# Kernel tuning notes

Measured on AMD Instinct MI355X. Metric: run time of the kernel, lower is better.

## Reference

```python
import jax, jax.numpy as jnp
import numpy as np

B, S, D = 4, 2048, 1024
H, DK, DV = 16, 64, 64
TEMP = (4 * DK) ** 0.5
EPS = 1e-6


def setup_inputs() -> dict:
    key = jax.random.key(0)
    ks = jax.random.split(key, 16)
    def lin(k, fin, fout):
        # torch Linear default init: U(-1/sqrt(fin), 1/sqrt(fin)); weight stored [fout,fin], we use [fin,fout]
        bound = 1.0 / np.sqrt(fin)
        return jax.random.uniform(k, (fin, fout), jnp.float32, -bound, bound)
    inp = {}
    for i, name in enumerate(['q_a', 'k_a', 'v_a', 'q_s', 'k_s', 'v_s']):
        inp[name] = jax.random.normal(ks[i], (B, S, D), jnp.float32)
    inp['Wqa'] = lin(ks[6], D, H * DK)
    inp['Wka'] = lin(ks[7], D, H * DK)
    inp['Wva'] = lin(ks[8], D, H * DV)
    inp['Wqs'] = lin(ks[9], D, H * DK)
    inp['Wks'] = lin(ks[10], D, H * DK)
    inp['Wvs'] = lin(ks[11], D, H * DV)
    inp['Wfc'] = lin(ks[12], H * DV, D)
    inp['gamma'] = jnp.ones((D,), jnp.float32)
    inp['beta'] = jnp.zeros((D,), jnp.float32)
    return inp


def _proj(x, W, dh):
    # [B,S,D] @ [D,H*dh] -> [B,H,S,dh]
    b, s, _ = x.shape
    return (x @ W).reshape(b, s, H, dh).transpose(0, 2, 1, 3)


def reference(q_a, k_a, v_a, q_s, k_s, v_s, Wqa, Wka, Wva, Wqs, Wks, Wvs, Wfc, gamma, beta):
    residual = q_a + q_s
    qa = _proj(q_a, Wqa, DK)
    ka = _proj(k_a, Wka, DK)
    va = _proj(v_a, Wva, DV)
    qs = _proj(q_s, Wqs, DK)
    ks = _proj(k_s, Wks, DK)
    vs = _proj(v_s, Wvs, DV)
    # a2a + a2s + s2a + s2s == (qa+qs) @ (ka+ks)^T  (same math, single GEMM)
    scores = jnp.einsum('bhqd,bhkd->bhqk', qa + qs, ka + ks) / TEMP
    attn = jax.nn.softmax(scores, axis=-1)  # [B,H,S,S]
    ctx = jnp.einsum('bhqk,bhkd->bhqd', attn, va + vs)
    ctx = ctx.transpose(0, 2, 1, 3).reshape(q_a.shape[0], q_a.shape[1], H * DV)
    out = ctx @ Wfc + residual
    mu = jnp.mean(out, axis=-1, keepdims=True)
    var = jnp.var(out, axis=-1, keepdims=True)
    out = (out - mu) * jax.lax.rsqrt(var + EPS) * gamma + beta
    return out
```

## Files before the change

### kernel.cpp

```cpp
#include <hip/hip_runtime.h>
#include <hip/hip_bf16.h>
#include <cstdint>
#include <cstddef>

typedef __bf16 bf16;
typedef __bf16 bf16x8 __attribute__((ext_vector_type(8)));
typedef __bf16 bf16x4v __attribute__((ext_vector_type(4)));
typedef __bf16 bf16x2v __attribute__((ext_vector_type(2)));
typedef float f32x4 __attribute__((ext_vector_type(4)));
typedef float f32x16 __attribute__((ext_vector_type(16)));
typedef unsigned uint2v __attribute__((ext_vector_type(2)));
typedef unsigned uint4v __attribute__((ext_vector_type(4)));

#define MFMA16(a, b, c) __builtin_amdgcn_mfma_f32_16x16x32_bf16((a), (b), (c), 0, 0, 0)
#define MFMA32(a, b, c) __builtin_amdgcn_mfma_f32_32x32x16_bf16((a), (b), (c), 0, 0, 0)
#define SWZ(row, byte) ((((row) * 128) + (byte)) ^ (((row) & 7) << 4))
#define GLOAD_LDS(g, l) \
    __builtin_amdgcn_global_load_lds((const __attribute__((address_space(1))) void*)(g), \
                                     (__attribute__((address_space(3))) void*)(l), 16, 0, 0)

constexpr int BB = 4, SS = 2048, DD = 1024, HH = 16;
constexpr int NROWS = BB * SS;
constexpr size_t NB = (size_t)NROWS * DD;
constexpr size_t NW = (size_t)DD * DD;

static __device__ __forceinline__ unsigned pk2(float a, float b) {
    bf16x2v h;
    h[0] = (bf16)a; h[1] = (bf16)b;
    return __builtin_bit_cast(unsigned, h);
}

static __device__ __forceinline__ bf16x8 frag4(unsigned w0, unsigned w1, unsigned w2, unsigned w3) {
    uint4v u;
    u[0] = w0; u[1] = w1; u[2] = w2; u[3] = w3;
    return __builtin_bit_cast(bf16x8, u);
}

struct Ptrs6 { const float* p[6]; };

__global__ __launch_bounds__(256) void cvt_in_kernel(Ptrs6 src, bf16* dst) {
    const int z = blockIdx.y;
    const size_t idx = (size_t)blockIdx.x * 256 + threadIdx.x;
    float4 v = ((const float4*)src.p[z])[idx];
    bf16x4v o;
    o[0] = (bf16)v.x; o[1] = (bf16)v.y; o[2] = (bf16)v.z; o[3] = (bf16)v.w;
    *(bf16x4v*)(dst + z * NB + idx * 4) = o;
}

struct Ptrs7 { const float* p[7]; };

__global__ __launch_bounds__(256) void cvt_w_kernel(Ptrs7 src, bf16* dst) {
    const int z = blockIdx.z;
    const float* W = src.p[z];
    bf16* WT = dst + (size_t)z * NW;
    __shared__ float tile[32][33];
    const int tx = threadIdx.x, ty = threadIdx.y;
    const int kb = blockIdx.y * 32, nb = blockIdx.x * 32;
#pragma unroll
    for (int j = 0; j < 4; ++j)
        tile[ty + j * 8][tx] = W[(size_t)(kb + ty + j * 8) * DD + nb + tx];
    __syncthreads();
#pragma unroll
    for (int j = 0; j < 4; ++j)
        WT[(size_t)(nb + ty + j * 8) * DD + kb + tx] = (bf16)tile[tx][ty + j * 8];
}

__global__ __launch_bounds__(256) void vt_kernel(const bf16* __restrict__ V,
                                                 bf16* __restrict__ Vt) {
    const int bh = blockIdx.y;
    const int s0 = blockIdx.x * 64;
    __shared__ bf16 t[64][72];
    const int tid = threadIdx.x;
    const int row = tid >> 2, seg = tid & 3;
    const bf16* src = V + ((size_t)bh * SS + s0 + row) * 64 + seg * 16;
    bf16x8 v0 = *(const bf16x8*)src;
    bf16x8 v1 = *(const bf16x8*)(src + 8);
#pragma unroll
    for (int j = 0; j < 8; ++j) {
        t[seg * 16 + j][row] = v0[j];
        t[seg * 16 + 8 + j][row] = v1[j];
    }
    __syncthreads();
    const int d = tid >> 2, c = (tid & 3) * 16;
    bf16x8 o0 = *(const bf16x8*)(&t[d][c]);
    bf16x8 o1 = *(const bf16x8*)(&t[d][c + 8]);
    bf16* dst = Vt + ((size_t)bh * 64 + d) * SS + s0 + c;
    *(bf16x8*)dst = o0;
    *(bf16x8*)(dst + 8) = o1;
}

struct GemmPtrs {
    const bf16* a1[3]; const bf16* a2[3];
    const bf16* b1[3]; const bf16* b2[3];
    bf16* outbh[3];
};

template <int MODE>
__global__ __launch_bounds__(256) void gemm_kernel(GemmPtrs P, int iters, int split,
                                                   float* outF, const float* r1, const float* r2) {
    const int cpx = gridDim.x >> 3;
    const int bid0 = blockIdx.x;
    const int work = (bid0 & 7) * cpx + (bid0 >> 3);
    const int z = work >> 9;
    const int rem = work & 511;
    const int m0 = (rem >> 3) * 128, n0 = (rem & 7) * 128;

    const bf16* __restrict__ A1 = P.a1[z];
    const bf16* __restrict__ A2 = P.a2[z];
    const bf16* __restrict__ B1 = P.b1[z];
    const bf16* __restrict__ B2 = P.b2[z];

    const int tid = threadIdx.x;
    const int lane = tid & 63, w = tid >> 6;
    const int g = lane >> 4, i = lane & 15;
    const int mb = (w >> 1) * 64, nb = (w & 1) * 64;

    __shared__ __align__(16) bf16 As[128 * 64];
    __shared__ __align__(16) bf16 Bs[128 * 64];

    const int lrow = lane >> 3, lseg = lane & 7;
    const int chunk = lseg ^ lrow;

    f32x4 acc[4][4];
#pragma unroll
    for (int aa = 0; aa < 4; ++aa)
#pragma unroll
        for (int bb = 0; bb < 4; ++bb) acc[aa][bb] = 0.0f;

    for (int kt = 0; kt < iters; ++kt) {
        const bf16* Ag; const bf16* Bg; int koff;
        if (kt < split) { Ag = A1; Bg = B1; koff = kt * 64; }
        else            { Ag = A2; Bg = B2; koff = (kt - split) * 64; }

        __syncthreads();
#pragma unroll
        for (int c = 0; c < 4; ++c) {
            const int row = (w * 4 + c) * 8 + lrow;
            const bf16* ap;
            if (MODE == 0) {
                ap = Ag + (size_t)(m0 + row) * DD + koff + chunk * 8;
            } else {
                int gr = m0 + row;
                ap = Ag + ((size_t)((gr >> 11) * HH + (koff >> 6)) * SS + (gr & 2047)) * 64 + chunk * 8;
            }
            const bf16* bp = Bg + (size_t)(n0 + row) * DD + koff + chunk * 8;
            GLOAD_LDS(ap, As + (w * 4 + c) * 512);
            GLOAD_LDS(bp, Bs + (w * 4 + c) * 512);
        }
        __syncthreads();

#pragma unroll
        for (int f = 0; f < 2; ++f) {
            bf16x8 af[4], bff[4];
#pragma unroll
            for (int mt = 0; mt < 4; ++mt) {
                int row = mb + mt * 16 + i;
                af[mt] = *(const bf16x8*)((char*)As + SWZ(row, f * 64 + g * 16));
            }
#pragma unroll
            for (int nt = 0; nt < 4; ++nt) {
                int row = nb + nt * 16 + i;
                bff[nt] = *(const bf16x8*)((char*)Bs + SWZ(row, f * 64 + g * 16));
            }
#pragma unroll
            for (int mt = 0; mt < 4; ++mt)
#pragma unroll
                for (int nt = 0; nt < 4; ++nt)
                    acc[mt][nt] = MFMA16(af[mt], bff[nt], acc[mt][nt]);
        }
    }

    if (MODE == 0) {
        bf16* outQ = P.outbh[z];
#pragma unroll
        for (int mt = 0; mt < 4; ++mt)
#pragma unroll
            for (int nt = 0; nt < 4; ++nt) {
                int colg = n0 + nb + nt * 16 + i;
                int h = colg >> 6, d = colg & 63;
#pragma unroll
                for (int r = 0; r < 4; ++r) {
                    int rowg = m0 + mb + mt * 16 + g * 4 + r;
                    int b = rowg >> 11, s = rowg & 2047;
                    outQ[(((size_t)(b * HH + h)) * SS + s) * 64 + d] = (bf16)acc[mt][nt][r];
                }
            }
    } else {
#pragma unroll
        for (int mt = 0; mt < 4; ++mt)
#pragma unroll
            for (int nt = 0; nt < 4; ++nt) {
                int colg = n0 + nb + nt * 16 + i;
#pragma unroll
                for (int r = 0; r < 4; ++r) {
                    int rowg = m0 + mb + mt * 16 + g * 4 + r;
                    size_t off = (size_t)rowg * DD + colg;
                    outF[off] = acc[mt][nt][r] + r1[off] + r2[off];
                }
            }
    }
}

__global__ __launch_bounds__(512, 4) void attn_kernel(const bf16* __restrict__ Qg,
                                                      const bf16* __restrict__ Kg,
                                                      const bf16* __restrict__ Vt,
                                                      bf16* __restrict__ ctxh) {
    const int bid = blockIdx.x;
    const int bh = ((bid & 7) << 3) | (bid >> 6);
    const int qt = (bid >> 3) & 7;

    const int tid = threadIdx.x;
    const int lane = tid & 63, w = tid >> 6;
    const int hi = lane >> 5, q = lane & 31;

    __shared__ __align__(16) char smem[32768];

    const int qrow = qt * 256 + w * 32 + q;
    bf16x8 qf[4];
    {
        const bf16* qp = Qg + ((size_t)bh * SS + qrow) * 64;
#pragma unroll
        for (int c = 0; c < 4; ++c) {
            bf16x8 v = *(const bf16x8*)(qp + c * 16 + hi * 8);
#pragma unroll
            for (int e = 0; e < 8; ++e) v[e] = (bf16)((float)v[e] * 0.0625f);
            qf[c] = v;
        }
    }

    const int srow = tid >> 3, sseg = tid & 7;
    const bf16* kgp = Kg + (size_t)bh * SS * 64;
    const bf16* vgp = Vt + (size_t)bh * 64 * SS;
    const int sbyte = SWZ(srow, sseg * 16);

    bf16x8 kreg = *(const bf16x8*)(kgp + (size_t)srow * 64 + sseg * 8);
    bf16x8 vreg = *(const bf16x8*)(vgp + (size_t)srow * SS + sseg * 8);

    f32x16 o0 = {}, o1 = {};
    float m = -3e38f, l = 0.0f;

    for (int kt = 0; kt < SS / 64; ++kt) {
        char* kb_ = smem + (kt & 1) * 16384;
        char* vb_ = kb_ + 8192;
        *(bf16x8*)(kb_ + sbyte) = kreg;
        *(bf16x8*)(vb_ + sbyte) = vreg;
        if (kt + 1 < SS / 64) {
            const int k0n = (kt + 1) * 64;
            kreg = *(const bf16x8*)(kgp + (size_t)(k0n + srow) * 64 + sseg * 8);
            vreg = *(const bf16x8*)(vgp + (size_t)srow * SS + k0n + sseg * 8);
        }
        __syncthreads();

        f32x16 st0 = {}, st1 = {};
        __builtin_amdgcn_s_setprio(1);
#pragma unroll
        for (int c = 0; c < 4; ++c) {
            bf16x8 kf = *(const bf16x8*)(kb_ + SWZ(q, c * 32 + hi * 16));
            st0 = MFMA32(kf, qf[c], st0);
        }
#pragma unroll
        for (int c = 0; c < 4; ++c) {
            bf16x8 kf = *(const bf16x8*)(kb_ + SWZ(32 + q, c * 32 + hi * 16));
            st1 = MFMA32(kf, qf[c], st1);
        }
        __builtin_amdgcn_s_setprio(0);

        float tm = st0[0];
#pragma unroll
        for (int r = 1; r < 16; ++r) tm = fmaxf(tm, st0[r]);
#pragma unroll
        for (int r = 0; r < 16; ++r) tm = fmaxf(tm, st1[r]);
        tm = fmaxf(tm, __shfl_xor(tm, 32, 64));
        if (!__all(tm - m <= 8.0f)) {
            float nm = fmaxf(m, tm);
            float al = __expf(m - nm);
            l *= al;
            o0 *= al;
            o1 *= al;
            m = nm;
        }
        float sum = 0.0f;
#pragma unroll
        for (int r = 0; r < 16; ++r) { st0[r] = __expf(st0[r] - m); sum += st0[r]; }
#pragma unroll
        for (int r = 0; r < 16; ++r) { st1[r] = __expf(st1[r] - m); sum += st1[r]; }
        l += sum;

        bf16x8 pf[4];
#pragma unroll
        for (int c = 0; c < 4; ++c) {
            const f32x16 s_ = (c < 2) ? st0 : st1;
            const int b0 = (c & 1) * 8;
            unsigned a0 = pk2(s_[b0 + 0], s_[b0 + 1]);
            unsigned c0 = pk2(s_[b0 + 4], s_[b0 + 5]);
            unsigned a1 = pk2(s_[b0 + 2], s_[b0 + 3]);
            unsigned c1 = pk2(s_[b0 + 6], s_[b0 + 7]);
            uint2v s1 = __builtin_amdgcn_permlane32_swap(a0, c0, false, false);
            uint2v s2 = __builtin_amdgcn_permlane32_swap(a1, c1, false, false);
            pf[c] = frag4(s1[0], s2[0], s1[1], s2[1]);
        }

        __builtin_amdgcn_s_setprio(1);
#pragma unroll
        for (int c = 0; c < 4; ++c) {
            bf16x8 vf = *(const bf16x8*)(vb_ + SWZ(q, c * 32 + hi * 16));
            o0 = MFMA32(vf, pf[c], o0);
        }
#pragma unroll
        for (int c = 0; c < 4; ++c) {
            bf16x8 vf = *(const bf16x8*)(vb_ + SWZ(32 + q, c * 32 + hi * 16));
            o1 = MFMA32(vf, pf[c], o1);
        }
        __builtin_amdgcn_s_setprio(0);
    }

    float lt = l + __shfl_xor(l, 32, 64);
    float rl = 1.0f / lt;
    __syncthreads();
    const int orow = w * 32 + q;
#pragma unroll
    for (int dh = 0; dh < 2; ++dh) {
#pragma unroll
        for (int r = 0; r < 16; r += 2) {
            float v0 = (dh ? o1[r] : o0[r]) * rl;
            float v1 = (dh ? o1[r + 1] : o0[r + 1]) * rl;
            int d = dh * 32 + (r & 3) + 8 * (r >> 2) + 4 * hi;
            *(unsigned*)(smem + SWZ(orow, d * 2)) = pk2(v0, v1);
        }
    }
    __syncthreads();
    {
        const int row = tid >> 1, hf = tid & 1;
        bf16* outp = ctxh + ((size_t)bh * SS + qt * 256 + row) * 64 + hf * 32;
#pragma unroll
        for (int c = 0; c < 4; ++c) {
            bf16x8 v = *(const bf16x8*)(smem + SWZ(row, hf * 64 + c * 16));
            *(bf16x8*)(outp + c * 8) = v;
        }
    }
}

__global__ __launch_bounds__(256) void ln_kernel(const float* __restrict__ tmp,
                                                 const float* __restrict__ gamma,
                                                 const float* __restrict__ beta,
                                                 float* __restrict__ out) {
    const int row = blockIdx.x;
    const int t = threadIdx.x;
    float4 v = ((const float4*)(tmp + (size_t)row * DD))[t];
    float s = v.x + v.y + v.z + v.w;
    float ss = v.x * v.x + v.y * v.y + v.z * v.z + v.w * v.w;
#pragma unroll
    for (int mask = 1; mask <= 32; mask <<= 1) {
        s += __shfl_xor(s, mask, 64);
        ss += __shfl_xor(ss, mask, 64);
    }
    __shared__ float red[8];
    const int w = t >> 6, lane = t & 63;
    if (lane == 0) { red[w] = s; red[4 + w] = ss; }
    __syncthreads();
    s = red[0] + red[1] + red[2] + red[3];
    ss = red[4] + red[5] + red[6] + red[7];
    const float mu = s * (1.0f / 1024.0f);
    const float var = ss * (1.0f / 1024.0f) - mu * mu;
    const float rs = rsqrtf(var + 1e-6f);
    float4 gm = ((const float4*)gamma)[t];
    float4 bt = ((const float4*)beta)[t];
    float4 ov;
    ov.x = (v.x - mu) * rs * gm.x + bt.x;
    ov.y = (v.y - mu) * rs * gm.y + bt.y;
    ov.z = (v.z - mu) * rs * gm.z + bt.z;
    ov.w = (v.w - mu) * rs * gm.w + bt.w;
    ((float4*)(out + (size_t)row * DD))[t] = ov;
}

extern "C" void kernel_launch(void* const* d_in, const int* in_sizes, int n_in,
                              void* d_out, int out_size, void* d_ws, size_t ws_size,
                              hipStream_t stream) {
    (void)in_sizes; (void)n_in; (void)out_size; (void)ws_size;

    char* ws = (char*)d_ws;
    bf16* xb = (bf16*)ws;
    bf16* wT = (bf16*)(ws + 100663296ull);
    bf16* Qg = (bf16*)(ws + 115343360ull);
    bf16* Kg = (bf16*)(ws + 132120576ull);
    bf16* Vg = (bf16*)(ws + 148897792ull);
    bf16* ctxh = (bf16*)ws;
    bf16* Vtg = (bf16*)(ws + 16777216ull);
    float* tmp = (float*)(ws + 33554432ull);

    {
        Ptrs6 p;
        for (int j = 0; j < 6; ++j) p.p[j] = (const float*)d_in[j];
        cvt_in_kernel<<<dim3(8192, 6), 256, 0, stream>>>(p, xb);
    }
    {
        Ptrs7 p;
        for (int j = 0; j < 7; ++j) p.p[j] = (const float*)d_in[6 + j];
        cvt_w_kernel<<<dim3(32, 32, 7), dim3(32, 8), 0, stream>>>(p, wT);
    }
    {
        GemmPtrs gp;
        gp.a1[0] = xb;           gp.a1[1] = xb + NB;     gp.a1[2] = xb + 2 * NB;
        gp.a2[0] = xb + 3 * NB;  gp.a2[1] = xb + 4 * NB; gp.a2[2] = xb + 5 * NB;
        gp.b1[0] = wT;           gp.b1[1] = wT + NW;     gp.b1[2] = wT + 2 * NW;
        gp.b2[0] = wT + 3 * NW;  gp.b2[1] = wT + 4 * NW; gp.b2[2] = wT + 5 * NW;
        gp.outbh[0] = Qg; gp.outbh[1] = Kg; gp.outbh[2] = Vg;
        gemm_kernel<0><<<dim3(1536), 256, 0, stream>>>(gp, 32, 16, nullptr, nullptr, nullptr);
    }
    vt_kernel<<<dim3(32, 64), 256, 0, stream>>>(Vg, Vtg);
    attn_kernel<<<dim3(512), 512, 0, stream>>>(Qg, Kg, Vtg, ctxh);
    {
        GemmPtrs gp;
        for (int j = 0; j < 3; ++j) {
            gp.a1[j] = ctxh; gp.a2[j] = ctxh;
            gp.b1[j] = wT + 6 * NW; gp.b2[j] = wT + 6 * NW;
            gp.outbh[j] = nullptr;
        }
        gemm_kernel<1><<<dim3(512), 256, 0, stream>>>(gp, 16, 16, tmp,
                                                      (const float*)d_in[0],
                                                      (const float*)d_in[3]);
    }
    ln_kernel<<<dim3(8192), 256, 0, stream>>>(tmp, (const float*)d_in[13],
                                              (const float*)d_in[14], (float*)d_out);
}
```

Measured before the change: 533.0 us.

## Replace QKV projection GEMM with 256x256-tile double-buffered 8-wave kernel

Replaces the 128x128-tile projection GEMM (1536 blocks of 256 threads) with a new 256x256-tile kernel (384 blocks of 512 threads). The new kernel stages A and B through 128 KB of double-buffered LDS with direct global-to-LDS loads and splits each K step into four phases. Each phase interleaves the next tile's loads with MFMA bursts, using explicit waitcnt, barriers and setprio. The larger tile cuts global and LDS traffic per FLOP, but the 128 KB of LDS per block and the many barriers limit occupancy, and 384 blocks may fill the CUs unevenly.

```diff
diff --git a/kernel.cpp b/kernel.cpp
--- a/kernel.cpp
+++ b/kernel.cpp
@@ -18,6 +18,10 @@
 #define GLOAD_LDS(g, l) \
     __builtin_amdgcn_global_load_lds((const __attribute__((address_space(1))) void*)(g), \
                                      (__attribute__((address_space(3))) void*)(l), 16, 0, 0)
+#define VMWAIT(n) asm volatile("s_waitcnt vmcnt(" #n ")" ::: "memory")
+#define LGKM0()   asm volatile("s_waitcnt lgkmcnt(0)" ::: "memory")
+#define BAR()     __builtin_amdgcn_s_barrier()
+#define SCHED0()  __builtin_amdgcn_sched_barrier(0)
 
 constexpr int BB = 4, SS = 2048, DD = 1024, HH = 16;
 constexpr int NROWS = BB * SS;
@@ -94,6 +98,164 @@
     const bf16* b1[3]; const bf16* b2[3];
     bf16* outbh[3];
 };
+
+__global__ __launch_bounds__(512, 2) void gemm256_kernel(GemmPtrs P) {
+    const int tid = threadIdx.x;
+    const int lane = tid & 63, w = tid >> 6;
+    const int g = lane >> 4, i = lane & 15;
+    const int chunk = (tid & 7) ^ ((tid >> 3) & 7);
+
+    const int cpx = gridDim.x >> 3;
+    const int work = (blockIdx.x & 7) * cpx + (blockIdx.x >> 3);
+    const int mpanel = work / 12;
+    const int ntile = work - mpanel * 12;
+    const int z = ntile >> 2;
+    const int n0 = (ntile & 3) * 256;
+    const int m0 = mpanel * 256;
+
+    const bf16* __restrict__ A1 = P.a1[z];
+    const bf16* __restrict__ A2 = P.a2[z];
+    const bf16* __restrict__ B1 = P.b1[z];
+    const bf16* __restrict__ B2 = P.b2[z];
+
+    __shared__ __align__(16) char smem[131072];
+
+    f32x4 acc[16][2];
+#pragma unroll
+    for (int a = 0; a < 16; ++a) { acc[a][0] = 0.0f; acc[a][1] = 0.0f; }
+
+    auto stage = [&](char* region, const bf16* G, int rc0, int rbase, int ko) {
+        GLOAD_LDS(G + (size_t)(rc0 + rbase + (tid >> 3)) * 1024 + ko + chunk * 8,
+                  region + rbase * 128 + w * 1024);
+    };
+
+#define LDFRAG(base, row, byte) (*(const bf16x8*)((base) + SWZ((row), (byte))))
+#define LDB_ALL(Bb) do { \
+    bf_[0][0] = LDFRAG((Bb), w * 32 + i,      g * 16); \
+    bf_[0][1] = LDFRAG((Bb), w * 32 + i,      64 + g * 16); \
+    bf_[1][0] = LDFRAG((Bb), w * 32 + 16 + i, g * 16); \
+    bf_[1][1] = LDFRAG((Bb), w * 32 + 16 + i, 64 + g * 16); } while (0)
+#define LDA_PH(Ab, q) do { \
+    af_[0][0] = LDFRAG((Ab), (q) * 64 + i,      g * 16); \
+    af_[0][1] = LDFRAG((Ab), (q) * 64 + i,      64 + g * 16); \
+    af_[1][0] = LDFRAG((Ab), (q) * 64 + 16 + i, g * 16); \
+    af_[1][1] = LDFRAG((Ab), (q) * 64 + 16 + i, 64 + g * 16); \
+    af_[2][0] = LDFRAG((Ab), (q) * 64 + 32 + i, g * 16); \
+    af_[2][1] = LDFRAG((Ab), (q) * 64 + 32 + i, 64 + g * 16); \
+    af_[3][0] = LDFRAG((Ab), (q) * 64 + 48 + i, g * 16); \
+    af_[3][1] = LDFRAG((Ab), (q) * 64 + 48 + i, 64 + g * 16); } while (0)
+#define MFMA_PH(q) do { \
+    __builtin_amdgcn_s_setprio(1); \
+    acc[(q)*4+0][0] = MFMA16(af_[0][0], bf_[0][0], acc[(q)*4+0][0]); \
+    acc[(q)*4+0][0] = MFMA16(af_[0][1], bf_[0][1], acc[(q)*4+0][0]); \
+    acc[(q)*4+0][1] = MFMA16(af_[0][0], bf_[1][0], acc[(q)*4+0][1]); \
+    acc[(q)*4+0][1] = MFMA16(af_[0][1], bf_[1][1], acc[(q)*4+0][1]); \
+    acc[(q)*4+1][0] = MFMA16(af_[1][0], bf_[0][0], acc[(q)*4+1][0]); \
+    acc[(q)*4+1][0] = MFMA16(af_[1][1], bf_[0][1], acc[(q)*4+1][0]); \
+    acc[(q)*4+1][1] = MFMA16(af_[1][0], bf_[1][0], acc[(q)*4+1][1]); \
+    acc[(q)*4+1][1] = MFMA16(af_[1][1], bf_[1][1], acc[(q)*4+1][1]); \
+    acc[(q)*4+2][0] = MFMA16(af_[2][0], bf_[0][0], acc[(q)*4+2][0]); \
+    acc[(q)*4+2][0] = MFMA16(af_[2][1], bf_[0][1], acc[(q)*4+2][0]); \
+    acc[(q)*4+2][1] = MFMA16(af_[2][0], bf_[1][0], acc[(q)*4+2][1]); \
+    acc[(q)*4+2][1] = MFMA16(af_[2][1], bf_[1][1], acc[(q)*4+2][1]); \
+    acc[(q)*4+3][0] = MFMA16(af_[3][0], bf_[0][0], acc[(q)*4+3][0]); \
+    acc[(q)*4+3][0] = MFMA16(af_[3][1], bf_[0][1], acc[(q)*4+3][0]); \
+    acc[(q)*4+3][1] = MFMA16(af_[3][0], bf_[1][0], acc[(q)*4+3][1]); \
+    acc[(q)*4+3][1] = MFMA16(af_[3][1], bf_[1][1], acc[(q)*4+3][1]); \
+    __builtin_amdgcn_s_setprio(0); } while (0)
+
+    stage(smem + 65536, B1, n0, 0, 0);
+    stage(smem + 65536, B1, n0, 64, 0);
+    stage(smem + 65536, B1, n0, 128, 0);
+    stage(smem + 65536, B1, n0, 192, 0);
+    stage(smem, A1, m0, 0, 0);
+    stage(smem, A1, m0, 64, 0);
+    stage(smem, A1, m0, 128, 0);
+    stage(smem, A1, m0, 192, 0);
+    VMWAIT(3);
+    BAR();
+
+    bf16x8 bf_[2][2], af_[4][2];
+
+    for (int t = 0; t < 31; ++t) {
+        const int cur = t & 1;
+        char* Ab = smem + cur * 32768;
+        char* Bb = smem + 65536 + cur * 32768;
+        char* An_ = smem + (cur ^ 1) * 32768;
+        char* Bn_ = smem + 65536 + (cur ^ 1) * 32768;
+        const int ts = t + 1;
+        const bf16* Ag; const bf16* Bg; int ko;
+        if (ts < 16) { Ag = A1; Bg = B1; ko = ts * 64; }
+        else         { Ag = A2; Bg = B2; ko = (ts - 16) * 64; }
+
+        LDB_ALL(Bb);
+        LDA_PH(Ab, 0);
+        stage(Bn_, Bg, n0, 0, ko);
+        stage(Bn_, Bg, n0, 64, ko);
+        VMWAIT(4); BAR(); LGKM0(); SCHED0();
+        MFMA_PH(0);
+        BAR();
+        LDA_PH(Ab, 1);
+        stage(Bn_, Bg, n0, 128, ko);
+        stage(Bn_, Bg, n0, 192, ko);
+        VMWAIT(5); BAR(); LGKM0(); SCHED0();
+        MFMA_PH(1);
+        BAR();
+        LDA_PH(Ab, 2);
+        stage(An_, Ag, m0, 0, ko);
+        stage(An_, Ag, m0, 64, ko);
+        VMWAIT(6); BAR(); LGKM0(); SCHED0();
+        MFMA_PH(2);
+        BAR();
+        LDA_PH(Ab, 3);
+        stage(An_, Ag, m0, 128, ko);
+        stage(An_, Ag, m0, 192, ko);
+        VMWAIT(3); BAR(); LGKM0(); SCHED0();
+        MFMA_PH(3);
+        BAR();
+    }
+
+    {
+        char* Ab = smem + 32768;
+        char* Bb = smem + 65536 + 32768;
+        LDB_ALL(Bb);
+        LDA_PH(Ab, 0);
+        VMWAIT(2); BAR(); LGKM0(); SCHED0();
+        MFMA_PH(0);
+        BAR();
+        LDA_PH(Ab, 1);
+        VMWAIT(1); BAR(); LGKM0(); SCHED0();
+        MFMA_PH(1);
+        BAR();
+        LDA_PH(Ab, 2);
+        VMWAIT(0); BAR(); LGKM0(); SCHED0();
+        MFMA_PH(2);
+        BAR();
+        LDA_PH(Ab, 3);
+        LGKM0(); SCHED0();
+        MFMA_PH(3);
+    }
+
+    bf16* outQ = P.outbh[z];
+#pragma unroll
+    for (int mt = 0; mt < 16; ++mt) {
+#pragma unroll
+        for (int nt = 0; nt < 2; ++nt) {
+            int c = n0 + w * 32 + nt * 16 + i;
+            int h = c >> 6, d = c & 63;
+#pragma unroll
+            for (int r = 0; r < 4; ++r) {
+                int rowg = m0 + mt * 16 + g * 4 + r;
+                int b = rowg >> 11, s = rowg & 2047;
+                outQ[(((size_t)(b * HH + h)) * SS + s) * 64 + d] = (bf16)acc[mt][nt][r];
+            }
+        }
+    }
+#undef LDFRAG
+#undef LDB_ALL
+#undef LDA_PH
+#undef MFMA_PH
+}
 
 template <int MODE>
 __global__ __launch_bounds__(256) void gemm_kernel(GemmPtrs P, int iters, int split,
@@ -405,7 +567,7 @@
         gp.b1[0] = wT;           gp.b1[1] = wT + NW;     gp.b1[2] = wT + 2 * NW;
         gp.b2[0] = wT + 3 * NW;  gp.b2[1] = wT + 4 * NW; gp.b2[2] = wT + 5 * NW;
         gp.outbh[0] = Qg; gp.outbh[1] = Kg; gp.outbh[2] = Vg;
-        gemm_kernel<0><<<dim3(1536), 256, 0, stream>>>(gp, 32, 16, nullptr, nullptr, nullptr);
+        gemm256_kernel<<<dim3(384), 512, 0, stream>>>(gp);
     }
     vt_kernel<<<dim3(32, 64), 256, 0, stream>>>(Vg, Vtg);
     attn_kernel<<<dim3(512), 512, 0, stream>>>(Qg, Kg, Vtg, ctxh);
```

After: 523.6 us. No clear change (-1.8%).

## Rewrite projection GEMMs with 256x128 tiles and triple-buffered async LDS pipeline

Applied to the files above, without the earlier changes.

Replaces the synchronous single-buffer GEMM with a 512-thread, 256x128-tile kernel that keeps three LDS stages in flight using global_load_lds. Tile t+2 is prefetched while tile t is computed, with explicit vmcnt/lgkmcnt waits, barriers and raised MFMA priority. The aim is to hide global-load latency and halve B-tile reloads per output. In exchange it needs 144KB of LDS per block, which limits occupancy, and depends on delicate hand-placed waits.

```diff
diff --git a/kernel.cpp b/kernel.cpp
--- a/kernel.cpp
+++ b/kernel.cpp
@@ -18,6 +18,10 @@
 #define GLOAD_LDS(g, l) \
     __builtin_amdgcn_global_load_lds((const __attribute__((address_space(1))) void*)(g), \
                                      (__attribute__((address_space(3))) void*)(l), 16, 0, 0)
+#define VMWAIT(n) asm volatile("s_waitcnt vmcnt(" #n ")" ::: "memory")
+#define LGKM0()   asm volatile("s_waitcnt lgkmcnt(0)" ::: "memory")
+#define BAR()     __builtin_amdgcn_s_barrier()
+#define SCHED0()  __builtin_amdgcn_sched_barrier(0)
 
 constexpr int BB = 4, SS = 2048, DD = 1024, HH = 16;
 constexpr int NROWS = BB * SS;
@@ -95,107 +99,160 @@
     bf16* outbh[3];
 };
 
-template <int MODE>
-__global__ __launch_bounds__(256) void gemm_kernel(GemmPtrs P, int iters, int split,
-                                                   float* outF, const float* r1, const float* r2) {
+template <int MODE, int NNT>
+__global__ __launch_bounds__(512, 2) void gemm_dp_kernel(GemmPtrs P, int iters, int split,
+                                                         float* outF, const float* r1,
+                                                         const float* r2) {
+    const int tid = threadIdx.x;
+    const int lane = tid & 63, w = tid >> 6;
+    const int g = lane >> 4, i = lane & 15;
+    const int chunk = (tid & 7) ^ ((tid >> 3) & 7);
+    const int mw = w >> 1, nw = w & 1;
+
     const int cpx = gridDim.x >> 3;
-    const int bid0 = blockIdx.x;
-    const int work = (bid0 & 7) * cpx + (bid0 >> 3);
-    const int z = work >> 9;
-    const int rem = work & 511;
-    const int m0 = (rem >> 3) * 128, n0 = (rem & 7) * 128;
+    const int work = (blockIdx.x & 7) * cpx + (blockIdx.x >> 3);
+    const int mpanel = work / NNT;
+    const int nt = work - mpanel * NNT;
+    const int z = nt >> 3;
+    const int n0 = (nt & 7) * 128;
+    const int m0 = mpanel * 256;
 
     const bf16* __restrict__ A1 = P.a1[z];
     const bf16* __restrict__ A2 = P.a2[z];
     const bf16* __restrict__ B1 = P.b1[z];
     const bf16* __restrict__ B2 = P.b2[z];
 
-    const int tid = threadIdx.x;
-    const int lane = tid & 63, w = tid >> 6;
-    const int g = lane >> 4, i = lane & 15;
-    const int mb = (w >> 1) * 64, nb = (w & 1) * 64;
-
-    __shared__ __align__(16) bf16 As[128 * 64];
-    __shared__ __align__(16) bf16 Bs[128 * 64];
-
-    const int lrow = lane >> 3, lseg = lane & 7;
-    const int chunk = lseg ^ lrow;
+    __shared__ __align__(16) char smem[147456];
 
     f32x4 acc[4][4];
 #pragma unroll
-    for (int aa = 0; aa < 4; ++aa)
-#pragma unroll
-        for (int bb = 0; bb < 4; ++bb) acc[aa][bb] = 0.0f;
-
-    for (int kt = 0; kt < iters; ++kt) {
-        const bf16* Ag; const bf16* Bg; int koff;
-        if (kt < split) { Ag = A1; Bg = B1; koff = kt * 64; }
-        else            { Ag = A2; Bg = B2; koff = (kt - split) * 64; }
-
-        __syncthreads();
-#pragma unroll
-        for (int c = 0; c < 4; ++c) {
-            const int row = (w * 4 + c) * 8 + lrow;
-            const bf16* ap;
-            if (MODE == 0) {
-                ap = Ag + (size_t)(m0 + row) * DD + koff + chunk * 8;
-            } else {
-                int gr = m0 + row;
-                ap = Ag + ((size_t)((gr >> 11) * HH + (koff >> 6)) * SS + (gr & 2047)) * 64 + chunk * 8;
-            }
-            const bf16* bp = Bg + (size_t)(n0 + row) * DD + koff + chunk * 8;
-            GLOAD_LDS(ap, As + (w * 4 + c) * 512);
-            GLOAD_LDS(bp, Bs + (w * 4 + c) * 512);
-        }
-        __syncthreads();
-
-#pragma unroll
-        for (int f = 0; f < 2; ++f) {
-            bf16x8 af[4], bff[4];
-#pragma unroll
-            for (int mt = 0; mt < 4; ++mt) {
-                int row = mb + mt * 16 + i;
-                af[mt] = *(const bf16x8*)((char*)As + SWZ(row, f * 64 + g * 16));
-            }
-#pragma unroll
-            for (int nt = 0; nt < 4; ++nt) {
-                int row = nb + nt * 16 + i;
-                bff[nt] = *(const bf16x8*)((char*)Bs + SWZ(row, f * 64 + g * 16));
-            }
-#pragma unroll
-            for (int mt = 0; mt < 4; ++mt)
-#pragma unroll
-                for (int nt = 0; nt < 4; ++nt)
-                    acc[mt][nt] = MFMA16(af[mt], bff[nt], acc[mt][nt]);
-        }
-    }
+    for (int a = 0; a < 4; ++a)
+#pragma unroll
+        for (int b = 0; b < 4; ++b) acc[a][b] = 0.0f;
+
+    auto stageA = [&](char* buf, const bf16* Ag, int rbase, int ko) {
+        const int gr = m0 + rbase + (tid >> 3);
+        const bf16* ap;
+        if (MODE == 0) {
+            ap = Ag + (size_t)gr * 1024 + ko + chunk * 8;
+        } else {
+            ap = Ag + ((size_t)((gr >> 11) * HH + (ko >> 6)) * SS + (gr & 2047)) * 64 + chunk * 8;
+        }
+        GLOAD_LDS(ap, buf + rbase * 128 + w * 1024);
+    };
+    auto stageB = [&](char* buf, const bf16* Bg, int rbase, int ko) {
+        const bf16* bp = Bg + (size_t)(n0 + rbase + (tid >> 3)) * 1024 + ko + chunk * 8;
+        GLOAD_LDS(bp, buf + 32768 + rbase * 128 + w * 1024);
+    };
+    auto stage_tile = [&](int ts, char* buf) {
+        const bf16* Ag; const bf16* Bg; int ko;
+        if (ts < split) { Ag = A1; Bg = B1; ko = ts * 64; }
+        else            { Ag = A2; Bg = B2; ko = (ts - split) * 64; }
+        stageA(buf, Ag, 0, ko);
+        stageA(buf, Ag, 64, ko);
+        stageA(buf, Ag, 128, ko);
+        stageA(buf, Ag, 192, ko);
+        stageB(buf, Bg, 0, ko);
+        stageB(buf, Bg, 64, ko);
+    };
+
+    bf16x8 af_[4], bf_[4];
+
+#define LDFRAGS(bufc, kf) do { \
+    char* Ab_ = (bufc); char* Bb_ = (bufc) + 32768; \
+    af_[0] = *(const bf16x8*)(Ab_ + SWZ(mw * 64 +  0 + i, (kf) * 64 + g * 16)); \
+    af_[1] = *(const bf16x8*)(Ab_ + SWZ(mw * 64 + 16 + i, (kf) * 64 + g * 16)); \
+    af_[2] = *(const bf16x8*)(Ab_ + SWZ(mw * 64 + 32 + i, (kf) * 64 + g * 16)); \
+    af_[3] = *(const bf16x8*)(Ab_ + SWZ(mw * 64 + 48 + i, (kf) * 64 + g * 16)); \
+    bf_[0] = *(const bf16x8*)(Bb_ + SWZ(nw * 64 +  0 + i, (kf) * 64 + g * 16)); \
+    bf_[1] = *(const bf16x8*)(Bb_ + SWZ(nw * 64 + 16 + i, (kf) * 64 + g * 16)); \
+    bf_[2] = *(const bf16x8*)(Bb_ + SWZ(nw * 64 + 32 + i, (kf) * 64 + g * 16)); \
+    bf_[3] = *(const bf16x8*)(Bb_ + SWZ(nw * 64 + 48 + i, (kf) * 64 + g * 16)); \
+} while (0)
+
+#define DO_MFMA() do { \
+    __builtin_amdgcn_s_setprio(1); \
+    _Pragma("unroll") \
+    for (int mt = 0; mt < 4; ++mt) \
+        _Pragma("unroll") \
+        for (int nn = 0; nn < 4; ++nn) \
+            acc[mt][nn] = MFMA16(af_[mt], bf_[nn], acc[mt][nn]); \
+    __builtin_amdgcn_s_setprio(0); \
+} while (0)
+
+    stage_tile(0, smem);
+    stage_tile(1, smem + 49152);
+    VMWAIT(6);
+    BAR();
+
+    int bufsel = 0, stagesel = 2;
+    for (int t = 0; t < iters - 2; ++t) {
+        char* buf = smem + bufsel * 49152;
+        LDFRAGS(buf, 0);
+        stage_tile(t + 2, smem + stagesel * 49152);
+        BAR(); LGKM0(); SCHED0();
+        DO_MFMA();
+        BAR();
+        LDFRAGS(buf, 1);
+        VMWAIT(6);
+        BAR(); LGKM0(); SCHED0();
+        DO_MFMA();
+        BAR();
+        bufsel = (bufsel == 2) ? 0 : bufsel + 1;
+        stagesel = (stagesel == 2) ? 0 : stagesel + 1;
+    }
+    {
+        char* buf = smem + bufsel * 49152;
+        LDFRAGS(buf, 0);
+        BAR(); LGKM0(); SCHED0();
+        DO_MFMA();
+        BAR();
+        LDFRAGS(buf, 1);
+        VMWAIT(0);
+        BAR(); LGKM0(); SCHED0();
+        DO_MFMA();
+        BAR();
+        bufsel = (bufsel == 2) ? 0 : bufsel + 1;
+    }
+    {
+        char* buf = smem + bufsel * 49152;
+        LDFRAGS(buf, 0);
+        BAR(); LGKM0(); SCHED0();
+        DO_MFMA();
+        BAR();
+        LDFRAGS(buf, 1);
+        LGKM0(); SCHED0();
+        DO_MFMA();
+    }
+#undef LDFRAGS
+#undef DO_MFMA
 
     if (MODE == 0) {
         bf16* outQ = P.outbh[z];
 #pragma unroll
         for (int mt = 0; mt < 4; ++mt)
 #pragma unroll
-            for (int nt = 0; nt < 4; ++nt) {
-                int colg = n0 + nb + nt * 16 + i;
-                int h = colg >> 6, d = colg & 63;
+            for (int nn = 0; nn < 4; ++nn) {
+                int c = n0 + nw * 64 + nn * 16 + i;
+                int h = c >> 6, d = c & 63;
 #pragma unroll
                 for (int r = 0; r < 4; ++r) {
-                    int rowg = m0 + mb + mt * 16 + g * 4 + r;
+                    int rowg = m0 + mw * 64 + mt * 16 + g * 4 + r;
                     int b = rowg >> 11, s = rowg & 2047;
-                    outQ[(((size_t)(b * HH + h)) * SS + s) * 64 + d] = (bf16)acc[mt][nt][r];
+                    outQ[(((size_t)(b * HH + h)) * SS + s) * 64 + d] = (bf16)acc[mt][nn][r];
                 }
             }
     } else {
 #pragma unroll
         for (int mt = 0; mt < 4; ++mt)
 #pragma unroll
-            for (int nt = 0; nt < 4; ++nt) {
-                int colg = n0 + nb + nt * 16 + i;
+            for (int nn = 0; nn < 4; ++nn) {
+                int colg = n0 + nw * 64 + nn * 16 + i;
 #pragma unroll
                 for (int r = 0; r < 4; ++r) {
-                    int rowg = m0 + mb + mt * 16 + g * 4 + r;
+                    int rowg = m0 + mw * 64 + mt * 16 + g * 4 + r;
                     size_t off = (size_t)rowg * DD + colg;
-                    outF[off] = acc[mt][nt][r] + r1[off] + r2[off];
+                    outF[off] = acc[mt][nn][r] + r1[off] + r2[off];
                 }
             }
     }
@@ -405,7 +462,7 @@
         gp.b1[0] = wT;           gp.b1[1] = wT + NW;     gp.b1[2] = wT + 2 * NW;
         gp.b2[0] = wT + 3 * NW;  gp.b2[1] = wT + 4 * NW; gp.b2[2] = wT + 5 * NW;
         gp.outbh[0] = Qg; gp.outbh[1] = Kg; gp.outbh[2] = Vg;
-        gemm_kernel<0><<<dim3(1536), 256, 0, stream>>>(gp, 32, 16, nullptr, nullptr, nullptr);
+        gemm_dp_kernel<0, 24><<<dim3(768), 512, 0, stream>>>(gp, 32, 16, nullptr, nullptr, nullptr);
     }
     vt_kernel<<<dim3(32, 64), 256, 0, stream>>>(Vg, Vtg);
     attn_kernel<<<dim3(512), 512, 0, stream>>>(Qg, Kg, Vtg, ctxh);
@@ -416,9 +473,9 @@
             gp.b1[j] = wT + 6 * NW; gp.b2[j] = wT + 6 * NW;
             gp.outbh[j] = nullptr;
         }
-        gemm_kernel<1><<<dim3(512), 256, 0, stream>>>(gp, 16, 16, tmp,
-                                                      (const float*)d_in[0],
-                                                      (const float*)d_in[3]);
+        gemm_dp_kernel<1, 8><<<dim3(256), 512, 0, stream>>>(gp, 16, 16, tmp,
+                                                            (const float*)d_in[0],
+                                                            (const float*)d_in[3]);
     }
     ln_kernel<<<dim3(8192), 256, 0, stream>>>(tmp, (const float*)d_in[13],
                                               (const float*)d_in[14], (float*)d_out);
```

Result: faster. 511.5 us (-4.0%).
